# Optimization experiments

Measured on AMD Instinct MI355X. Metric: run time of the kernel, lower is better.

## Reference

```python
import jax, jax.numpy as jnp
import numpy as np

D = 1536          # model dim
N = 12            # num heads
HD = D // N       # head dim = 128
C = HD // 2       # rope complex channels = 64
F, H, W = 4, 32, 32
L = F * H * W     # 4096 tokens
B = 1
S1 = C - 2 * (C // 3)   # 22 channels for the frame axis
S2 = C // 3             # 21 channels each for h and w axes
EPS = 1e-6


def setup_inputs() -> dict:
    key = jax.random.key(0)
    ks = jax.random.split(key, 9)
    sc = 1.0 / np.sqrt(D)
    inp = {"x": jax.random.normal(ks[0], (B, L, D), jnp.float32)}
    for i, name in enumerate(["wq", "wk", "wv", "wo"]):
        inp[name] = jax.random.normal(ks[1 + i], (D, D), jnp.float32) * sc
    for i, name in enumerate(["bq", "bk", "bv", "bo"]):
        inp[name] = jax.random.normal(ks[5 + i], (D,), jnp.float32) * 0.01
    inp["gq"] = jnp.ones((D,), jnp.float32)
    inp["gk"] = jnp.ones((D,), jnp.float32)
    # precomputed rotary tables: angle[pos, j] = pos * theta_j (complex freqs = cos + i sin)
    pos = jnp.arange(1024, dtype=jnp.float32)
    inv = 10000.0 ** (-jnp.arange(C, dtype=jnp.float32) / C)
    ang = pos[:, None] * inv[None, :]
    inp["freqs_cos"] = jnp.cos(ang)
    inp["freqs_sin"] = jnp.sin(ang)
    inp["seq_lens"] = jnp.full((B,), L, dtype=jnp.int32)
    inp["f_size"] = F
    inp["h_size"] = H
    inp["w_size"] = W
    return inp


def _rms(y, g):
    return y * jax.lax.rsqrt(jnp.mean(y * y, axis=-1, keepdims=True) + EPS) * g


def _grid(tab, f, h, w):
    # concat per-axis frequency bands: [f,h,w, S1 | S2 | rest] -> [L, 1, C]
    a = jnp.broadcast_to(tab[:f, None, None, :S1], (f, h, w, S1))
    b = jnp.broadcast_to(tab[None, :h, None, S1:S1 + S2], (f, h, w, S2))
    c = jnp.broadcast_to(tab[None, None, :w, S1 + S2:], (f, h, w, C - S1 - S2))
    return jnp.concatenate([a, b, c], axis=-1).reshape(f * h * w, 1, C)


def reference(x, wq, bq, wk, bk, wv, bv, wo, bo, gq, gk,
              freqs_cos, freqs_sin, seq_lens, f_size, h_size, w_size):
    b, l, dim = x.shape
    n = N
    d = dim // n
    c = d // 2
    # QKV projections with QK RMSNorm (norm over full model dim, as in the module)
    q = _rms(x @ wq.T + bq, gq).reshape(b, l, n, d)
    k = _rms(x @ wk.T + bk, gk).reshape(b, l, n, d)
    v = (x @ wv.T + bv).reshape(b, l, n, d)
    # 3D rotary: complex multiply by per-position grid frequencies
    cosg = _grid(freqs_cos, f_size, h_size, w_size)  # [L,1,C]
    sing = _grid(freqs_sin, f_size, h_size, w_size)

    def rope(t):
        tr = t.reshape(b, l, n, c, 2)
        xr, xi = tr[..., 0], tr[..., 1]
        return jnp.stack([xr * cosg - xi * sing, xr * sing + xi * cosg], axis=-1).reshape(b, l, n, d)

    q = rope(q)
    k = rope(k)
    # full (non-windowed) scaled dot-product attention, all k_lens == L
    scores = jnp.einsum('blnd,bmnd->bnlm', q, k) / jnp.sqrt(jnp.float32(d))
    attn = jax.nn.softmax(scores, axis=-1)
    out = jnp.einsum('bnlm,bmnd->blnd', attn, v).reshape(b, l, dim)
    return out @ wo.T + bo
```

## Files before the change

kernel.cpp:

```cpp
#include <hip/hip_runtime.h>
#include <math.h>

#define Dm   1536
#define NHd  12
#define HDm  128
#define Ltok 4096
#define S1c  22
#define S2c  21
#define MFIX 5.0f
#define LOG2E 1.4426950408889634f

typedef __attribute__((ext_vector_type(8))) _Float16 f16x8;
typedef __attribute__((ext_vector_type(4))) float f32x4;

static __device__ __forceinline__ f32x4 MFMA16(f16x8 a, f16x8 b, f32x4 c) {
  return __builtin_amdgcn_mfma_f32_16x16x32_f16(a, b, c, 0, 0, 0);
}

static __device__ __forceinline__ unsigned int pack_f16(float a, float b) {
  union { _Float16 h[2]; unsigned int u; } x;
  x.h[0] = (_Float16)a; x.h[1] = (_Float16)b;
  return x.u;
}

static __device__ __forceinline__ void gload_lds16(const void* g, void* l) {
  __builtin_amdgcn_global_load_lds(
      (const __attribute__((address_space(1))) unsigned int*)g,
      (__attribute__((address_space(3))) unsigned int*)l, 16, 0, 0);
}

__global__ __launch_bounds__(256) void cvt_f16(
    const float* __restrict__ src, unsigned short* __restrict__ dst, int nslots)
{
  int i = blockIdx.x * 256 + threadIdx.x;
  if (i >= nslots) return;
  float4 v = *(const float4*)&src[(size_t)i * 4];
  uint2 p;
  p.x = pack_f16(v.x, v.y);
  p.y = pack_f16(v.z, v.w);
  *(uint2*)&dst[(size_t)i * 4] = p;
}

__global__ __launch_bounds__(256) void cvt_w4_f16(
    const float* __restrict__ w0, const float* __restrict__ w1,
    const float* __restrict__ w2, const float* __restrict__ w3,
    unsigned short* __restrict__ dst)
{
  const int which = blockIdx.y;
  const float* src = (which == 0) ? w0 : (which == 1) ? w1 : (which == 2) ? w2 : w3;
  unsigned short* d = dst + (size_t)which * Dm * Dm;
  int i = blockIdx.x * 256 + threadIdx.x;
  float4 v = *(const float4*)&src[(size_t)i * 4];
  uint2 p;
  p.x = pack_f16(v.x, v.y);
  p.y = pack_f16(v.z, v.w);
  *(uint2*)&d[(size_t)i * 4] = p;
}

__global__ __launch_bounds__(256) void gemm_qkv_f16(
    const unsigned short* __restrict__ Ag, const unsigned short* __restrict__ Wg,
    const float* __restrict__ bq, const float* __restrict__ bk,
    const float* __restrict__ bv,
    float* __restrict__ qb, float* __restrict__ kb,
    unsigned short* __restrict__ vT)
{
  __shared__ __align__(16) unsigned short As[2][128][32], Bs[2][128][32];
  const int tid = threadIdx.x;
  const int w = tid >> 6, lane = tid & 63;
  const int nx = lane & 15, g = lane >> 4;
  const int m0 = blockIdx.y * 128, n0 = blockIdx.x * 128;
  const int wr = w >> 1, wc = w & 1;
  const int which = (n0 >= 2 * Dm) ? 2 : ((n0 >= Dm) ? 1 : 0);
  const int n0loc = n0 - which * Dm;

  const int srow = lane >> 2, scol = (lane & 3) * 8;
  const unsigned short* gp;
  char* lbase0;
  if (w < 2) {
    gp = Ag + (size_t)(m0 + w * 64 + srow) * Dm + scol;
    lbase0 = (char*)&As[0][0][0] + w * 4096;
  } else {
    gp = Wg + (size_t)(n0 + (w - 2) * 64 + srow) * Dm + scol;
    lbase0 = (char*)&Bs[0][0][0] + (w - 2) * 4096;
  }

  f32x4 acc[4][4];
#pragma unroll
  for (int i = 0; i < 4; i++)
#pragma unroll
    for (int j = 0; j < 4; j++) acc[i][j] = (f32x4){0.f, 0.f, 0.f, 0.f};

#pragma unroll
  for (int c = 0; c < 4; ++c)
    gload_lds16(gp + (size_t)c * 16 * Dm, lbase0 + c * 1024);
  gp += 32;

  const int NK = Dm / 32;
  for (int it = 0; it < NK; ++it) {
    const int cur = it & 1;
    if (it + 1 < NK) {
      char* lb = lbase0 + (cur ^ 1) * 8192;
#pragma unroll
      for (int c = 0; c < 4; ++c)
        gload_lds16(gp + (size_t)c * 16 * Dm, lb + c * 1024);
      gp += 32;
      asm volatile("s_waitcnt vmcnt(4)" ::: "memory");
    } else {
      asm volatile("s_waitcnt vmcnt(0)" ::: "memory");
    }
    __builtin_amdgcn_s_barrier();
    f16x8 ah[4], bh[4];
#pragma unroll
    for (int i = 0; i < 4; ++i) {
      ah[i] = *(const f16x8*)&As[cur][wr * 64 + i * 16 + nx][g * 8];
      bh[i] = *(const f16x8*)&Bs[cur][wc * 64 + i * 16 + nx][g * 8];
    }
#pragma unroll
    for (int i = 0; i < 4; ++i)
#pragma unroll
      for (int j = 0; j < 4; ++j)
        acc[i][j] = MFMA16(ah[i], bh[j], acc[i][j]);
    __builtin_amdgcn_s_barrier();
  }

  if (which < 2) {
    float* Cout = which ? kb : qb;
    const float* bias = which ? bk : bq;
#pragma unroll
    for (int j = 0; j < 4; ++j) {
      const int col = n0loc + wc * 64 + j * 16 + nx;
      const float bz = bias[col];
#pragma unroll
      for (int i = 0; i < 4; ++i) {
        const int row0 = m0 + wr * 64 + i * 16 + g * 4;
#pragma unroll
        for (int r = 0; r < 4; ++r)
          Cout[(size_t)(row0 + r) * Dm + col] = acc[i][j][r] + bz;
      }
    }
  } else {
#pragma unroll
    for (int j = 0; j < 4; ++j) {
      const int col = n0loc + wc * 64 + j * 16 + nx;
      const float bz = bv[col];
#pragma unroll
      for (int i = 0; i < 4; ++i) {
        const int row0 = m0 + wr * 64 + i * 16 + g * 4;
        uint2 pk;
        pk.x = pack_f16(acc[i][j][0] + bz, acc[i][j][1] + bz);
        pk.y = pack_f16(acc[i][j][2] + bz, acc[i][j][3] + bz);
        *(uint2*)&vT[(size_t)col * Ltok + row0] = pk;
      }
    }
  }
}

__global__ __launch_bounds__(256) void gemm_nt_f16(
    const unsigned short* __restrict__ Ag, const unsigned short* __restrict__ Wg,
    const float* __restrict__ bias, float* __restrict__ Cout)
{
  __shared__ __align__(16) unsigned short As[2][128][32], Bs[2][128][32];
  const int tid = threadIdx.x;
  const int w = tid >> 6, lane = tid & 63;
  const int nx = lane & 15, g = lane >> 4;
  const int m0 = blockIdx.y * 128, n0 = blockIdx.x * 128;
  const int wr = w >> 1, wc = w & 1;

  const int srow = lane >> 2, scol = (lane & 3) * 8;
  const unsigned short* gp;
  char* lbase0;
  if (w < 2) {
    gp = Ag + (size_t)(m0 + w * 64 + srow) * Dm + scol;
    lbase0 = (char*)&As[0][0][0] + w * 4096;
  } else {
    gp = Wg + (size_t)(n0 + (w - 2) * 64 + srow) * Dm + scol;
    lbase0 = (char*)&Bs[0][0][0] + (w - 2) * 4096;
  }

  f32x4 acc[4][4];
#pragma unroll
  for (int i = 0; i < 4; i++)
#pragma unroll
    for (int j = 0; j < 4; j++) acc[i][j] = (f32x4){0.f, 0.f, 0.f, 0.f};

#pragma unroll
  for (int c = 0; c < 4; ++c)
    gload_lds16(gp + (size_t)c * 16 * Dm, lbase0 + c * 1024);
  gp += 32;

  const int NK = Dm / 32;
  for (int it = 0; it < NK; ++it) {
    const int cur = it & 1;
    if (it + 1 < NK) {
      char* lb = lbase0 + (cur ^ 1) * 8192;
#pragma unroll
      for (int c = 0; c < 4; ++c)
        gload_lds16(gp + (size_t)c * 16 * Dm, lb + c * 1024);
      gp += 32;
      asm volatile("s_waitcnt vmcnt(4)" ::: "memory");
    } else {
      asm volatile("s_waitcnt vmcnt(0)" ::: "memory");
    }
    __builtin_amdgcn_s_barrier();
    f16x8 ah[4], bh[4];
#pragma unroll
    for (int i = 0; i < 4; ++i) {
      ah[i] = *(const f16x8*)&As[cur][wr * 64 + i * 16 + nx][g * 8];
      bh[i] = *(const f16x8*)&Bs[cur][wc * 64 + i * 16 + nx][g * 8];
    }
#pragma unroll
    for (int i = 0; i < 4; ++i)
#pragma unroll
      for (int j = 0; j < 4; ++j)
        acc[i][j] = MFMA16(ah[i], bh[j], acc[i][j]);
    __builtin_amdgcn_s_barrier();
  }
#pragma unroll
  for (int j = 0; j < 4; ++j) {
    const int col = n0 + wc * 64 + j * 16 + nx;
    const float bz = bias[col];
#pragma unroll
    for (int i = 0; i < 4; ++i) {
      const int row0 = m0 + wr * 64 + i * 16 + g * 4;
#pragma unroll
      for (int r = 0; r < 4; ++r)
        Cout[(size_t)(row0 + r) * Dm + col] = acc[i][j][r] + bz;
    }
  }
}

__global__ __launch_bounds__(256) void rmsnorm_rope_f16(
    float* __restrict__ q, float* __restrict__ k,
    const float* __restrict__ gq, const float* __restrict__ gk,
    const float* __restrict__ fcos, const float* __restrict__ fsin)
{
  const int l = blockIdx.x;
  const int tid = threadIdx.x;
  const int d0 = tid * 6;
  float qv[6], kv[6];
  float sq = 0.f, sk = 0.f;
  const float* qp = &q[(size_t)l * Dm + d0];
  const float* kp = &k[(size_t)l * Dm + d0];
#pragma unroll
  for (int i = 0; i < 6; i++) {
    qv[i] = qp[i]; sq += qv[i] * qv[i];
    kv[i] = kp[i]; sk += kv[i] * kv[i];
  }
#pragma unroll
  for (int s = 1; s < 64; s <<= 1) {
    sq += __shfl_xor(sq, s);
    sk += __shfl_xor(sk, s);
  }
  __shared__ float redq[4], redk[4];
  if ((tid & 63) == 0) { redq[tid >> 6] = sq; redk[tid >> 6] = sk; }
  __syncthreads();
  sq = redq[0] + redq[1] + redq[2] + redq[3];
  sk = redk[0] + redk[1] + redk[2] + redk[3];
  const float rq = rsqrtf(sq * (1.f / (float)Dm) + 1e-6f);
  const float rk = rsqrtf(sk * (1.f / (float)Dm) + 1e-6f);
  const float qscale = 0.08838834764831845f * LOG2E;
  const int f = l >> 10, h = (l >> 5) & 31, w = l & 31;
  unsigned short* qo = (unsigned short*)q + (size_t)l * Dm;
  unsigned short* ko = (unsigned short*)k + (size_t)l * Dm;
#pragma unroll
  for (int i = 0; i < 3; i++) {
    const int d = d0 + 2 * i;
    const int cc = (d & (HDm - 1)) >> 1;
    const int pos = (cc < S1c) ? f : ((cc < S1c + S2c) ? h : w);
    const float co = fcos[pos * 64 + cc];
    const float si = fsin[pos * 64 + cc];
    const float xr = qv[2 * i]     * rq * gq[d];
    const float xi = qv[2 * i + 1] * rq * gq[d + 1];
    *(unsigned int*)&qo[d] =
        pack_f16((xr * co - xi * si) * qscale, (xr * si + xi * co) * qscale);
    const float yr = kv[2 * i]     * rk * gk[d];
    const float yi = kv[2 * i + 1] * rk * gk[d + 1];
    *(unsigned int*)&ko[d] = pack_f16(yr * co - yi * si, yr * si + yi * co);
  }
}

__global__ __launch_bounds__(256, 3) void attn_f16(
    const unsigned short* __restrict__ qs, const unsigned short* __restrict__ ks,
    const unsigned short* __restrict__ vT,
    float* __restrict__ Op0, float* __restrict__ Op1,
    float* __restrict__ stats)
{
  __shared__ __align__(16) unsigned short Ks[2][32][136];
  __shared__ __align__(16) unsigned short Vs[2][128][40];
  __shared__ __align__(16) unsigned short Ps[4][32][40];

  const int tid = threadIdx.x;
  const int w = tid >> 6, lane = tid & 63;
  const int nx = lane & 15, g = lane >> 4;
  const int head = blockIdx.y;
  const int half = blockIdx.z;
  const int qbase = blockIdx.x * 128 + w * 32;
  const int kvbase = half * (Ltok / 2);
  float* __restrict__ Op = half ? Op1 : Op0;

  const float NEGMFIX2 = -MFIX * LOG2E;

  f16x8 vones;
#pragma unroll
  for (int i = 0; i < 8; i++) vones[i] = (_Float16)1.0f;

  f16x8 qf[2][4];
#pragma unroll
  for (int s = 0; s < 2; s++) {
    const unsigned short* qp =
        &qs[(size_t)(qbase + s * 16 + nx) * Dm + head * HDm + g * 8];
#pragma unroll
    for (int c = 0; c < 4; c++) qf[s][c] = *(const f16x8*)(qp + c * 32);
  }

  f32x4 oacc[2][9];
#pragma unroll
  for (int s = 0; s < 2; s++)
#pragma unroll
    for (int nt = 0; nt < 9; nt++) oacc[s][nt] = (f32x4){0.f, 0.f, 0.f, 0.f};

  const int krow = tid >> 3, kchb = (tid & 7) << 4;
  const int vrow = tid >> 1, vseg = (tid & 1) << 4;

  const unsigned short* kg = &ks[(size_t)(kvbase + krow) * Dm + head * HDm + kchb];
  const unsigned short* vg = &vT[((size_t)head * HDm + vrow) * Ltok + kvbase + vseg];

  {
    uint4 ka = *(const uint4*)kg, kb4 = *(const uint4*)(kg + 8);
    uint4 va = *(const uint4*)vg, vb4 = *(const uint4*)(vg + 8);
    *(uint4*)&Ks[0][krow][kchb]     = ka;
    *(uint4*)&Ks[0][krow][kchb + 8] = kb4;
    *(uint4*)&Vs[0][vrow][vseg]     = va;
    *(uint4*)&Vs[0][vrow][vseg + 8] = vb4;
  }
  __syncthreads();

  const int NIT = Ltok / 2 / 32;
  for (int t = 0; t < NIT; t++) {
    const int cur = t & 1, nxt = cur ^ 1;
    const bool pref = (t + 1 < NIT);
    uint4 ka, kb4, va, vb4;
    if (pref) {
      kg += 32 * Dm;
      vg += 32;
      ka  = *(const uint4*)kg;  kb4 = *(const uint4*)(kg + 8);
      va  = *(const uint4*)vg;  vb4 = *(const uint4*)(vg + 8);
    }

    f32x4 sa[2][2];
#pragma unroll
    for (int s = 0; s < 2; s++)
#pragma unroll
      for (int mt = 0; mt < 2; mt++)
        sa[s][mt] = (f32x4){NEGMFIX2, NEGMFIX2, NEGMFIX2, NEGMFIX2};
    __builtin_amdgcn_s_setprio(1);
#pragma unroll
    for (int c = 0; c < 4; c++) {
      f16x8 k0f = *(const f16x8*)&Ks[cur][nx][c * 32 + g * 8];
      f16x8 k1f = *(const f16x8*)&Ks[cur][16 + nx][c * 32 + g * 8];
#pragma unroll
      for (int s = 0; s < 2; s++) {
        sa[s][0] = MFMA16(k0f, qf[s][c], sa[s][0]);
        sa[s][1] = MFMA16(k1f, qf[s][c], sa[s][1]);
      }
    }
    __builtin_amdgcn_s_setprio(0);

#pragma unroll
    for (int s = 0; s < 2; s++) {
      float p[8];
#pragma unroll
      for (int r = 0; r < 4; r++) {
        p[r]     = __builtin_amdgcn_exp2f(sa[s][0][r]);
        p[4 + r] = __builtin_amdgcn_exp2f(sa[s][1][r]);
      }
#pragma unroll
      for (int mt = 0; mt < 2; mt++) {
        unsigned int u0 = pack_f16(p[4 * mt + 0], p[4 * mt + 1]);
        unsigned int u1 = pack_f16(p[4 * mt + 2], p[4 * mt + 3]);
        *(uint2*)&Ps[w][s * 16 + nx][mt * 16 + g * 4] = make_uint2(u0, u1);
      }
    }
    __builtin_amdgcn_sched_barrier(0);

    f16x8 ph[2];
#pragma unroll
    for (int s = 0; s < 2; s++)
      ph[s] = *(const f16x8*)&Ps[w][s * 16 + nx][g * 8];
    __builtin_amdgcn_s_setprio(1);
#pragma unroll
    for (int nt = 0; nt < 8; nt++) {
      f16x8 vh = *(const f16x8*)&Vs[cur][nt * 16 + nx][g * 8];
#pragma unroll
      for (int s = 0; s < 2; s++)
        oacc[s][nt] = MFMA16(ph[s], vh, oacc[s][nt]);
    }
#pragma unroll
    for (int s = 0; s < 2; s++)
      oacc[s][8] = MFMA16(ph[s], vones, oacc[s][8]);
    __builtin_amdgcn_s_setprio(0);

    if (pref) {
      *(uint4*)&Ks[nxt][krow][kchb]     = ka;
      *(uint4*)&Ks[nxt][krow][kchb + 8] = kb4;
      *(uint4*)&Vs[nxt][vrow][vseg]     = va;
      *(uint4*)&Vs[nxt][vrow][vseg + 8] = vb4;
    }
    __syncthreads();
  }

#pragma unroll
  for (int s = 0; s < 2; s++) {
#pragma unroll
    for (int nt = 0; nt < 8; nt++)
#pragma unroll
      for (int r = 0; r < 4; r++)
        Op[(size_t)(qbase + s * 16 + g * 4 + r) * Dm + head * HDm + nt * 16 + nx] =
            oacc[s][nt][r];
    if (nx == 0) {
#pragma unroll
      for (int r = 0; r < 4; r++)
        stats[((size_t)half * Ltok + qbase + s * 16 + g * 4 + r) * NHd + head] =
            oacc[s][8][r];
    }
  }
}

__global__ __launch_bounds__(384) void combine_f16(
    const float* __restrict__ Op0, const float* __restrict__ Op1,
    const float* __restrict__ stats, unsigned short* __restrict__ oh)
{
  const int row = blockIdx.x;
  const int c4 = threadIdx.x * 4;
  const int head = c4 >> 7;
  const float l0 = stats[(size_t)row * NHd + head];
  const float l1 = stats[((size_t)Ltok + row) * NHd + head];
  const float rl = 1.f / (l0 + l1);
  float4 o0 = *(const float4*)&Op0[(size_t)row * Dm + c4];
  float4 o1 = *(const float4*)&Op1[(size_t)row * Dm + c4];
  uint2 p;
  p.x = pack_f16((o0.x + o1.x) * rl, (o0.y + o1.y) * rl);
  p.y = pack_f16((o0.z + o1.z) * rl, (o0.w + o1.w) * rl);
  *(uint2*)&oh[(size_t)row * Dm + c4] = p;
}

extern "C" void kernel_launch(void* const* d_in, const int* in_sizes, int n_in,
                              void* d_out, int out_size, void* d_ws, size_t ws_size,
                              hipStream_t stream)
{
  const float* x    = (const float*)d_in[0];
  const float* wq   = (const float*)d_in[1];
  const float* wk   = (const float*)d_in[2];
  const float* wv   = (const float*)d_in[3];
  const float* wo   = (const float*)d_in[4];
  const float* bq   = (const float*)d_in[5];
  const float* bk   = (const float*)d_in[6];
  const float* bv   = (const float*)d_in[7];
  const float* bo   = (const float*)d_in[8];
  const float* gq   = (const float*)d_in[9];
  const float* gk   = (const float*)d_in[10];
  const float* fcos = (const float*)d_in[11];
  const float* fsin = (const float*)d_in[12];
  float* out = (float*)d_out;

  const size_t LD = (size_t)Ltok * Dm;
  const size_t WH = (size_t)Dm * Dm;
  float* base = (float*)d_ws;
  float* qb = base;
  float* kb = base + LD;
  unsigned short* vT  = (unsigned short*)(base + 2 * LD);
  unsigned short* xh  = (unsigned short*)(base + 2 * LD + LD / 2);
  float* Op0 = base + 2 * LD + LD / 2;
  float* Op1 = Op0 + LD;
  unsigned short* wqh = (unsigned short*)(Op1 + LD);
  unsigned short* woh = wqh + 3 * WH;
  unsigned short* oh  = (unsigned short*)base;
  float* stats = (float*)(wqh + 4 * WH);

  const int xslots = (int)(LD / 4);
  const int w4     = (int)(WH / 4);
  dim3 gqkv(3 * Dm / 128, Ltok / 128);
  dim3 gout(Dm / 128, Ltok / 128);

  cvt_f16<<<(xslots + 255) / 256, 256, 0, stream>>>(x, xh, xslots);
  cvt_w4_f16<<<dim3(w4 / 256, 4), 256, 0, stream>>>(wq, wk, wv, wo, wqh);

  gemm_qkv_f16<<<gqkv, 256, 0, stream>>>(xh, wqh, bq, bk, bv, qb, kb, vT);
  rmsnorm_rope_f16<<<Ltok, 256, 0, stream>>>(qb, kb, gq, gk, fcos, fsin);
  attn_f16<<<dim3(Ltok / 128, NHd, 2), 256, 0, stream>>>(
      (const unsigned short*)qb, (const unsigned short*)kb, vT, Op0, Op1, stats);
  combine_f16<<<Ltok, 384, 0, stream>>>(Op0, Op1, stats, oh);
  gemm_nt_f16<<<gout, 256, 0, stream>>>(oh, woh, bo, out);
}
```

Before: 394.6 us.

## Keep softmax probabilities in registers by permuting V layout in shared memory

Removes the per-wave LDS round-trip for the probability tile (store P, barrier, reload as MFMA operand). The exp2 outputs are packed directly into the f16x8 A operand. V columns are stored in shared memory with a matching permutation so the key index order lines up with the register layout of the score accumulator. This saves LDS traffic and a scheduling barrier per iteration. In exchange, V stores become four 8-byte writes instead of two 16-byte writes.

New measurement: 394.9 us. About the same (+0.1%).

```diff
diff --git a/kernel.cpp b/kernel.cpp
--- a/kernel.cpp
+++ b/kernel.cpp
@@ -287,7 +287,6 @@
 {
   __shared__ __align__(16) unsigned short Ks[2][32][136];
   __shared__ __align__(16) unsigned short Vs[2][128][40];
-  __shared__ __align__(16) unsigned short Ps[4][32][40];
 
   const int tid = threadIdx.x;
   const int w = tid >> 6, lane = tid & 63;
@@ -321,17 +320,25 @@
 
   const int krow = tid >> 3, kchb = (tid & 7) << 4;
   const int vrow = tid >> 1, vseg = (tid & 1) << 4;
+  const int vofs = (tid & 1) << 2;
 
   const unsigned short* kg = &ks[(size_t)(kvbase + krow) * Dm + head * HDm + kchb];
   const unsigned short* vg = &vT[((size_t)head * HDm + vrow) * Ltok + kvbase + vseg];
+
+#define VSTORE_PI(buf, va_, vb_)                                              \
+  {                                                                           \
+    *(uint2*)&Vs[buf][vrow][vofs]      = make_uint2((va_).x, (va_).y);        \
+    *(uint2*)&Vs[buf][vrow][8 + vofs]  = make_uint2((va_).z, (va_).w);        \
+    *(uint2*)&Vs[buf][vrow][16 + vofs] = make_uint2((vb_).x, (vb_).y);        \
+    *(uint2*)&Vs[buf][vrow][24 + vofs] = make_uint2((vb_).z, (vb_).w);        \
+  }
 
   {
     uint4 ka = *(const uint4*)kg, kb4 = *(const uint4*)(kg + 8);
     uint4 va = *(const uint4*)vg, vb4 = *(const uint4*)(vg + 8);
     *(uint4*)&Ks[0][krow][kchb]     = ka;
     *(uint4*)&Ks[0][krow][kchb + 8] = kb4;
-    *(uint4*)&Vs[0][vrow][vseg]     = va;
-    *(uint4*)&Vs[0][vrow][vseg + 8] = vb4;
+    VSTORE_PI(0, va, vb4);
   }
   __syncthreads();
 
@@ -366,6 +373,7 @@
     }
     __builtin_amdgcn_s_setprio(0);
 
+    union { unsigned int u[4]; f16x8 v; } ph[2];
 #pragma unroll
     for (int s = 0; s < 2; s++) {
       float p[8];
@@ -374,40 +382,33 @@
         p[r]     = __builtin_amdgcn_exp2f(sa[s][0][r]);
         p[4 + r] = __builtin_amdgcn_exp2f(sa[s][1][r]);
       }
-#pragma unroll
-      for (int mt = 0; mt < 2; mt++) {
-        unsigned int u0 = pack_f16(p[4 * mt + 0], p[4 * mt + 1]);
-        unsigned int u1 = pack_f16(p[4 * mt + 2], p[4 * mt + 3]);
-        *(uint2*)&Ps[w][s * 16 + nx][mt * 16 + g * 4] = make_uint2(u0, u1);
-      }
-    }
-    __builtin_amdgcn_sched_barrier(0);
-
-    f16x8 ph[2];
-#pragma unroll
-    for (int s = 0; s < 2; s++)
-      ph[s] = *(const f16x8*)&Ps[w][s * 16 + nx][g * 8];
+      ph[s].u[0] = pack_f16(p[0], p[1]);
+      ph[s].u[1] = pack_f16(p[2], p[3]);
+      ph[s].u[2] = pack_f16(p[4], p[5]);
+      ph[s].u[3] = pack_f16(p[6], p[7]);
+    }
+
     __builtin_amdgcn_s_setprio(1);
 #pragma unroll
     for (int nt = 0; nt < 8; nt++) {
       f16x8 vh = *(const f16x8*)&Vs[cur][nt * 16 + nx][g * 8];
 #pragma unroll
       for (int s = 0; s < 2; s++)
-        oacc[s][nt] = MFMA16(ph[s], vh, oacc[s][nt]);
+        oacc[s][nt] = MFMA16(ph[s].v, vh, oacc[s][nt]);
     }
 #pragma unroll
     for (int s = 0; s < 2; s++)
-      oacc[s][8] = MFMA16(ph[s], vones, oacc[s][8]);
+      oacc[s][8] = MFMA16(ph[s].v, vones, oacc[s][8]);
     __builtin_amdgcn_s_setprio(0);
 
     if (pref) {
       *(uint4*)&Ks[nxt][krow][kchb]     = ka;
       *(uint4*)&Ks[nxt][krow][kchb + 8] = kb4;
-      *(uint4*)&Vs[nxt][vrow][vseg]     = va;
-      *(uint4*)&Vs[nxt][vrow][vseg + 8] = vb4;
+      VSTORE_PI(nxt, va, vb4);
     }
     __syncthreads();
   }
+#undef VSTORE_PI
 
 #pragma unroll
   for (int s = 0; s < 2; s++) {
```
